# Kernel optimization log

Measured on AMD Instinct MI355X. Metric: run time of the kernel, lower is better.

Reference implementation:

```python
import jax, jax.numpy as jnp
import numpy as np

WS = 7          # window_size
NH = 4          # num_heads
C = 128         # channels
N = WS * WS     # tokens per window = 49
BW = 4096       # number of windows total (batch * windows_per_image)
NW = 64         # windows per image (mask leading dim)


def _rel_pos_index(ws):
    coords = np.stack(np.meshgrid(np.arange(ws), np.arange(ws), indexing='ij'))
    cf = coords.reshape(2, -1)
    rel = (cf[:, :, None] - cf[:, None, :]).transpose(1, 2, 0)
    rel[:, :, 0] += ws - 1
    rel[:, :, 1] += ws - 1
    rel[:, :, 0] *= 2 * ws - 1
    return jnp.asarray(rel.sum(-1).ravel(), dtype=jnp.int32)  # [N*N]


def setup_inputs() -> dict:
    key = jax.random.key(0)
    ks = jax.random.split(key, 6)
    x = jax.random.normal(ks[0], (BW, N, C), dtype=jnp.float32)
    qkv_w = jax.random.normal(ks[1], (C, 3 * C), dtype=jnp.float32) * 0.02
    qkv_b = jnp.zeros((3 * C,), dtype=jnp.float32)
    proj_w = jax.random.normal(ks[2], (C, C), dtype=jnp.float32) * 0.02
    proj_b = jnp.zeros((C,), dtype=jnp.float32)
    bias_table = jax.random.normal(ks[3], ((2 * WS - 1) ** 2, NH), dtype=jnp.float32) * 0.02
    # Swin shifted-window mask: 0 where attention allowed, -100 where blocked
    keep = jax.random.bernoulli(ks[4], 0.5, (NW, N, N))
    mask = jnp.where(keep, 0.0, -100.0).astype(jnp.float32)
    return {"x": x, "qkv_w": qkv_w, "qkv_b": qkv_b, "proj_w": proj_w,
            "proj_b": proj_b, "bias_table": bias_table, "mask": mask}


def reference(x, qkv_w, qkv_b, proj_w, proj_b, bias_table, mask):
    B_, n, c = x.shape
    h = NH
    d = c // h
    scale = d ** -0.5

    qkv = x @ qkv_w + qkv_b                       # [B_, N, 3C]
    qkv = qkv.reshape(B_, n, 3, h, d).transpose(2, 0, 3, 1, 4)  # [3, B_, h, N, d]
    q, k, v = qkv[0], qkv[1], qkv[2]

    attn = jnp.einsum('bhnd,bhmd->bhnm', q * scale, k)          # [B_, h, N, N]

    idx = _rel_pos_index(WS)
    rpb = bias_table[idx].reshape(n, n, h).transpose(2, 0, 1)   # [h, N, N]
    attn = attn + rpb[None]

    nW = mask.shape[0]
    attn = attn.reshape(-1, nW, h, n, n) + mask[None, :, None]  # [B, nW, h, N, N]
    attn = attn.reshape(-1, h, n, n)
    attn = jax.nn.softmax(attn, axis=-1)

    out = jnp.einsum('bhnm,bhmd->bhnd', attn, v)  # [B_, h, N, d]
    out = out.transpose(0, 2, 1, 3).reshape(B_, n, c)
    return out @ proj_w + proj_b
```

## Files before the change

### kernel.cpp

```cpp
#include <hip/hip_runtime.h>

#define NTOK 49
#define CH   128
#define NHEAD 4
#define SCALE 0.17677669529663687f

typedef __bf16 bf16x8 __attribute__((ext_vector_type(8)));
typedef short  s16x8  __attribute__((ext_vector_type(8)));
typedef float  f32x4  __attribute__((ext_vector_type(4)));
typedef s16x8 s16x8_a __attribute__((may_alias));
typedef unsigned short u16_a __attribute__((may_alias));

__device__ __forceinline__ unsigned short f2bf(float f) {
  unsigned int u = __builtin_bit_cast(unsigned int, f);
  u += 0x7FFFu + ((u >> 16) & 1u);
  return (unsigned short)(u >> 16);
}

__device__ __forceinline__ f32x4 mfma_bf16(s16x8 a, s16x8 b, f32x4 c) {
  return __builtin_amdgcn_mfma_f32_16x16x32_bf16(
      __builtin_bit_cast(bf16x8, a), __builtin_bit_cast(bf16x8, b), c, 0, 0, 0);
}

__global__ void prep_kernel(const float* __restrict__ qkv_w,
                            const float* __restrict__ proj_w,
                            const float* __restrict__ bias_table,
                            unsigned short* __restrict__ wT,
                            unsigned short* __restrict__ pT,
                            float* __restrict__ rpb) {
  int t = blockIdx.x * 256 + threadIdx.x;
  if (t < 384 * 128) {
    int n = t >> 7, k = t & 127;
    float v = qkv_w[k * 384 + n];
    if (n < 128) v *= SCALE;
    wT[n * 128 + k] = f2bf(v);
  } else if (t < 384 * 128 + 128 * 128) {
    int u = t - 384 * 128;
    int n = u >> 7, k = u & 127;
    pT[n * 128 + k] = f2bf(proj_w[k * 128 + n]);
  } else if (t < 384 * 128 + 128 * 128 + NHEAD * NTOK * NTOK) {
    int u = t - (384 * 128 + 128 * 128);
    int h = u / (NTOK * NTOK);
    int ij = u % (NTOK * NTOK);
    int i = ij / NTOK, j = ij % NTOK;
    int idx = (i / 7 - j / 7 + 6) * 13 + (i % 7 - j % 7 + 6);
    rpb[h * (NTOK * NTOK) + ij] = bias_table[idx * NHEAD + h];
  }
}

__global__ __launch_bounds__(256, 3)
void attn_fused_kernel(const float* __restrict__ x,
                       const float* __restrict__ qkv_b,
                       const float* __restrict__ proj_b,
                       const float* __restrict__ mask,
                       const unsigned short* __restrict__ wT,
                       const unsigned short* __restrict__ pT,
                       const float* __restrict__ rpb,
                       float* __restrict__ out) {
  __shared__ __align__(16) char smem_raw[52224];
  unsigned short* const smem = (unsigned short*)smem_raw;

  const int w    = blockIdx.x;
  const int tid  = threadIdx.x;
  const int wave = tid >> 6;
  const int lane = tid & 63;
  const int quad = lane >> 4;
  const int l16  = lane & 15;
  const int h    = wave;
  const int wq8  = quad * 8;

  unsigned short* const Xs   = smem;
  unsigned short* const priv = smem + 6656 + wave * 4864;
  unsigned short* const qs   = priv;
  unsigned short* const ks   = priv;
  unsigned short* const ps   = priv;
  unsigned short* const vt   = priv + 2560;
  unsigned short* const ao   = smem;

  const f32x4 fzero = {0.f, 0.f, 0.f, 0.f};

  {
    const float* xw = x + (size_t)w * (NTOK * CH);
    for (int t = tid; t < NTOK * 32; t += 256) {
      const int row = t >> 5;
      const int c4  = (t & 31) << 2;
      const float4 v = *(const float4*)(xw + row * CH + c4);
      ushort4 pk;
      pk.x = f2bf(v.x); pk.y = f2bf(v.y); pk.z = f2bf(v.z); pk.w = f2bf(v.w);
      *(ushort4*)(Xs + row * 136 + c4) = pk;
    }
  }
  __syncthreads();

  int xrow[4];
#pragma unroll
  for (int mt = 0; mt < 4; ++mt) {
    const int rr = mt * 16 + l16;
    xrow[mt] = (rr < NTOK ? rr : NTOK - 1) * 136;
  }

  f32x4 accq[4][2];
#pragma unroll
  for (int mt = 0; mt < 4; ++mt)
#pragma unroll
    for (int nt = 0; nt < 2; ++nt) accq[mt][nt] = fzero;
#pragma unroll
  for (int kt = 0; kt < 4; ++kt) {
    s16x8 a[4], bq[2];
#pragma unroll
    for (int mt = 0; mt < 4; ++mt)
      a[mt] = *(const s16x8*)(Xs + xrow[mt] + kt * 32 + wq8);
#pragma unroll
    for (int nt = 0; nt < 2; ++nt)
      bq[nt] = *(const s16x8*)(wT + (size_t)(h * 32 + nt * 16 + l16) * 128 + kt * 32 + wq8);
#pragma unroll
    for (int mt = 0; mt < 4; ++mt)
#pragma unroll
      for (int nt = 0; nt < 2; ++nt)
        accq[mt][nt] = mfma_bf16(a[mt], bq[nt], accq[mt][nt]);
  }
#pragma unroll
  for (int nt = 0; nt < 2; ++nt) {
    const int col = nt * 16 + l16;
    const float bq_ = qkv_b[h * 32 + col] * SCALE;
#pragma unroll
    for (int mt = 0; mt < 4; ++mt)
#pragma unroll
      for (int r = 0; r < 4; ++r)
        *(u16_a*)(qs + (mt * 16 + quad * 4 + r) * 40 + col) = f2bf(accq[mt][nt][r] + bq_);
  }
  asm volatile("" ::: "memory");
  s16x8 qf[4];
#pragma unroll
  for (int t4 = 0; t4 < 4; ++t4)
    qf[t4] = *(const s16x8_a*)(qs + (t4 * 16 + l16) * 40 + wq8);
  asm volatile("s_waitcnt lgkmcnt(0)" ::: "memory");
  __builtin_amdgcn_sched_barrier(0);

  f32x4 acck[4][2];
#pragma unroll
  for (int mt = 0; mt < 4; ++mt)
#pragma unroll
    for (int nt = 0; nt < 2; ++nt) acck[mt][nt] = fzero;
#pragma unroll
  for (int kt = 0; kt < 4; ++kt) {
    s16x8 a[4], bk[2];
#pragma unroll
    for (int mt = 0; mt < 4; ++mt)
      a[mt] = *(const s16x8*)(Xs + xrow[mt] + kt * 32 + wq8);
#pragma unroll
    for (int nt = 0; nt < 2; ++nt)
      bk[nt] = *(const s16x8*)(wT + (size_t)(128 + h * 32 + nt * 16 + l16) * 128 + kt * 32 + wq8);
#pragma unroll
    for (int mt = 0; mt < 4; ++mt)
#pragma unroll
      for (int nt = 0; nt < 2; ++nt)
        acck[mt][nt] = mfma_bf16(a[mt], bk[nt], acck[mt][nt]);
  }
#pragma unroll
  for (int nt = 0; nt < 2; ++nt) {
    const int col = nt * 16 + l16;
    const float bk_ = qkv_b[128 + h * 32 + col];
#pragma unroll
    for (int mt = 0; mt < 4; ++mt)
#pragma unroll
      for (int r = 0; r < 4; ++r)
        *(u16_a*)(ks + (mt * 16 + quad * 4 + r) * 40 + col) = f2bf(acck[mt][nt][r] + bk_);
  }
  asm volatile("" ::: "memory");
  s16x8 kf[4];
#pragma unroll
  for (int t4 = 0; t4 < 4; ++t4)
    kf[t4] = *(const s16x8_a*)(ks + (t4 * 16 + l16) * 40 + wq8);
  asm volatile("s_waitcnt lgkmcnt(0)" ::: "memory");
  __builtin_amdgcn_sched_barrier(0);

  f32x4 accv[4][2];
#pragma unroll
  for (int mt = 0; mt < 4; ++mt)
#pragma unroll
    for (int nt = 0; nt < 2; ++nt) accv[mt][nt] = fzero;
#pragma unroll
  for (int kt = 0; kt < 4; ++kt) {
    s16x8 a[4], bv[2];
#pragma unroll
    for (int mt = 0; mt < 4; ++mt)
      a[mt] = *(const s16x8*)(Xs + xrow[mt] + kt * 32 + wq8);
#pragma unroll
    for (int nt = 0; nt < 2; ++nt)
      bv[nt] = *(const s16x8*)(wT + (size_t)(256 + h * 32 + nt * 16 + l16) * 128 + kt * 32 + wq8);
#pragma unroll
    for (int mt = 0; mt < 4; ++mt)
#pragma unroll
      for (int nt = 0; nt < 2; ++nt)
        accv[mt][nt] = mfma_bf16(a[mt], bv[nt], accv[mt][nt]);
  }
#pragma unroll
  for (int nt = 0; nt < 2; ++nt) {
    const float bv_ = qkv_b[256 + h * 32 + nt * 16 + l16];
#pragma unroll
    for (int mt = 0; mt < 4; ++mt)
#pragma unroll
      for (int r = 0; r < 4; ++r) {
        const int row = mt * 16 + quad * 4 + r;
        const int col = nt * 16 + l16;
        *(u16_a*)(vt + col * 72 + row) = f2bf(accv[mt][nt][r] + bv_);
      }
  }

  f32x4 s[4][4];
#pragma unroll
  for (int mt = 0; mt < 4; ++mt)
#pragma unroll
    for (int nt = 0; nt < 4; ++nt)
      s[mt][nt] = mfma_bf16(qf[mt], kf[nt], fzero);

  const float* maskw = mask + (size_t)(w & 63) * (NTOK * NTOK);
  const float* rpbh  = rpb + h * (NTOK * NTOK);
  float rinv[4][4];
  unsigned int pHold[4][4];
#pragma unroll
  for (int mt = 0; mt < 4; ++mt) {
#pragma unroll
    for (int r = 0; r < 4; ++r) {
      const int i = mt * 16 + quad * 4 + r;
      float vals[4];
      float vmax = -1e30f;
#pragma unroll
      for (int nt = 0; nt < 4; ++nt) {
        const int j = nt * 16 + l16;
        float v = -1e30f;
        if (i < NTOK && j < NTOK) {
          const int ij = i * NTOK + j;
          v = s[mt][nt][r] + rpbh[ij] + maskw[ij];
        }
        vals[nt] = v;
        vmax = fmaxf(vmax, v);
      }
#pragma unroll
      for (int off = 1; off < 16; off <<= 1)
        vmax = fmaxf(vmax, __shfl_xor(vmax, off, 64));
      float rsum = 0.f;
#pragma unroll
      for (int nt = 0; nt < 4; ++nt) {
        const float e = __expf(vals[nt] - vmax);
        vals[nt] = e;
        rsum += e;
      }
#pragma unroll
      for (int off = 1; off < 16; off <<= 1)
        rsum += __shfl_xor(rsum, off, 64);
      rinv[mt][r] = 1.f / rsum;
      *(u16_a*)(ps + i * 40 + l16)      = f2bf(vals[0]);
      *(u16_a*)(ps + i * 40 + 16 + l16) = f2bf(vals[1]);
      pHold[mt][r] = (unsigned int)f2bf(vals[2]) | ((unsigned int)f2bf(vals[3]) << 16);
    }
  }

  f32x4 o[4][2];
#pragma unroll
  for (int mt = 0; mt < 4; ++mt)
#pragma unroll
    for (int nt = 0; nt < 2; ++nt) o[mt][nt] = fzero;
  {
    s16x8 pf[4], vf[2];
#pragma unroll
    for (int mt = 0; mt < 4; ++mt)
      pf[mt] = *(const s16x8_a*)(ps + (mt * 16 + l16) * 40 + wq8);
#pragma unroll
    for (int nt = 0; nt < 2; ++nt)
      vf[nt] = *(const s16x8_a*)(vt + (nt * 16 + l16) * 72 + wq8);
#pragma unroll
    for (int mt = 0; mt < 4; ++mt)
#pragma unroll
      for (int nt = 0; nt < 2; ++nt)
        o[mt][nt] = mfma_bf16(pf[mt], vf[nt], o[mt][nt]);
  }
  asm volatile("s_waitcnt lgkmcnt(0)" ::: "memory");
  __builtin_amdgcn_sched_barrier(0);
#pragma unroll
  for (int mt = 0; mt < 4; ++mt)
#pragma unroll
    for (int r = 0; r < 4; ++r) {
      const int i = mt * 16 + quad * 4 + r;
      *(u16_a*)(ps + i * 40 + l16)      = (unsigned short)(pHold[mt][r] & 0xFFFFu);
      *(u16_a*)(ps + i * 40 + 16 + l16) = (unsigned short)(pHold[mt][r] >> 16);
    }
  asm volatile("" ::: "memory");
  {
    s16x8 pf[4], vf[2];
#pragma unroll
    for (int mt = 0; mt < 4; ++mt)
      pf[mt] = *(const s16x8_a*)(ps + (mt * 16 + l16) * 40 + wq8);
#pragma unroll
    for (int nt = 0; nt < 2; ++nt)
      vf[nt] = *(const s16x8_a*)(vt + (nt * 16 + l16) * 72 + 32 + wq8);
#pragma unroll
    for (int mt = 0; mt < 4; ++mt)
#pragma unroll
      for (int nt = 0; nt < 2; ++nt)
        o[mt][nt] = mfma_bf16(pf[mt], vf[nt], o[mt][nt]);
  }

  __syncthreads();
#pragma unroll
  for (int mt = 0; mt < 4; ++mt)
#pragma unroll
    for (int nt = 0; nt < 2; ++nt)
#pragma unroll
      for (int r = 0; r < 4; ++r) {
        const int row = mt * 16 + quad * 4 + r;
        *(u16_a*)(ao + row * 136 + h * 32 + nt * 16 + l16) = f2bf(o[mt][nt][r] * rinv[mt][r]);
      }
  __syncthreads();

  f32x4 po[4][2];
#pragma unroll
  for (int mt = 0; mt < 4; ++mt)
#pragma unroll
    for (int nt = 0; nt < 2; ++nt) po[mt][nt] = fzero;
#pragma unroll
  for (int kt = 0; kt < 4; ++kt) {
    s16x8 a[4], b[2];
#pragma unroll
    for (int mt = 0; mt < 4; ++mt)
      a[mt] = *(const s16x8_a*)(ao + (mt * 16 + l16) * 136 + kt * 32 + wq8);
#pragma unroll
    for (int nt = 0; nt < 2; ++nt)
      b[nt] = *(const s16x8*)(pT + (size_t)(h * 32 + nt * 16 + l16) * 128 + kt * 32 + wq8);
#pragma unroll
    for (int mt = 0; mt < 4; ++mt)
#pragma unroll
      for (int nt = 0; nt < 2; ++nt)
        po[mt][nt] = mfma_bf16(a[mt], b[nt], po[mt][nt]);
  }
  float* outw = out + (size_t)w * (NTOK * CH);
#pragma unroll
  for (int nt = 0; nt < 2; ++nt) {
    const int col = h * 32 + nt * 16 + l16;
    const float pb = proj_b[col];
#pragma unroll
    for (int mt = 0; mt < 4; ++mt)
#pragma unroll
      for (int r = 0; r < 4; ++r) {
        const int row = mt * 16 + quad * 4 + r;
        if (row < NTOK) outw[row * CH + col] = po[mt][nt][r] + pb;
      }
  }
}

extern "C" void kernel_launch(void* const* d_in, const int* in_sizes, int n_in,
                              void* d_out, int out_size, void* d_ws, size_t ws_size,
                              hipStream_t stream) {
  (void)in_sizes; (void)n_in; (void)out_size; (void)ws_size;
  const float* x          = (const float*)d_in[0];
  const float* qkv_w      = (const float*)d_in[1];
  const float* qkv_b      = (const float*)d_in[2];
  const float* proj_w     = (const float*)d_in[3];
  const float* proj_b     = (const float*)d_in[4];
  const float* bias_table = (const float*)d_in[5];
  const float* mask       = (const float*)d_in[6];
  float* out = (float*)d_out;

  unsigned short* wT = (unsigned short*)d_ws;
  unsigned short* pT = wT + 384 * 128;
  float* rpb = (float*)(pT + 128 * 128);

  const int prep_items = 384 * 128 + 128 * 128 + NHEAD * NTOK * NTOK;
  prep_kernel<<<(prep_items + 255) / 256, 256, 0, stream>>>(qkv_w, proj_w, bias_table,
                                                            wT, pT, rpb);
  attn_fused_kernel<<<4096, 256, 0, stream>>>(x, qkv_b, proj_b, mask, wT, pT, rpb, out);
}
```

Measured before the change: 294.8 us.

## Load x fragments directly from global memory and drop shared staging

Removes the shared-memory staging of the window's input rows. Each wave now loads its MFMA A-fragments straight from global fp32 x and converts them to bf16 in registers, once each for the Q, K and V projections. This frees about 13 KB of LDS per block and removes a block-wide barrier, and launch bounds are raised to target 4 resident blocks per CU. In exchange, every wave re-reads the whole window's x from cache three times and repeats the fp32-to-bf16 conversion, which multiplies global/L2 load traffic and ALU work.

```diff
diff --git a/kernel.cpp b/kernel.cpp
--- a/kernel.cpp
+++ b/kernel.cpp
@@ -48,7 +48,7 @@
   }
 }
 
-__global__ __launch_bounds__(256, 3)
+__global__ __launch_bounds__(256, 4)
 void attn_fused_kernel(const float* __restrict__ x,
                        const float* __restrict__ qkv_b,
                        const float* __restrict__ proj_b,
@@ -57,7 +57,7 @@
                        const unsigned short* __restrict__ pT,
                        const float* __restrict__ rpb,
                        float* __restrict__ out) {
-  __shared__ __align__(16) char smem_raw[52224];
+  __shared__ __align__(16) char smem_raw[38912];
   unsigned short* const smem = (unsigned short*)smem_raw;
 
   const int w    = blockIdx.x;
@@ -69,8 +69,7 @@
   const int h    = wave;
   const int wq8  = quad * 8;
 
-  unsigned short* const Xs   = smem;
-  unsigned short* const priv = smem + 6656 + wave * 4864;
+  unsigned short* const priv = smem + wave * 4864;
   unsigned short* const qs   = priv;
   unsigned short* const ks   = priv;
   unsigned short* const ps   = priv;
@@ -79,24 +78,12 @@
 
   const f32x4 fzero = {0.f, 0.f, 0.f, 0.f};
 
-  {
-    const float* xw = x + (size_t)w * (NTOK * CH);
-    for (int t = tid; t < NTOK * 32; t += 256) {
-      const int row = t >> 5;
-      const int c4  = (t & 31) << 2;
-      const float4 v = *(const float4*)(xw + row * CH + c4);
-      ushort4 pk;
-      pk.x = f2bf(v.x); pk.y = f2bf(v.y); pk.z = f2bf(v.z); pk.w = f2bf(v.w);
-      *(ushort4*)(Xs + row * 136 + c4) = pk;
-    }
-  }
-  __syncthreads();
-
-  int xrow[4];
+  const float* xw = x + (size_t)w * (NTOK * CH);
+  int rofs[4];
 #pragma unroll
   for (int mt = 0; mt < 4; ++mt) {
     const int rr = mt * 16 + l16;
-    xrow[mt] = (rr < NTOK ? rr : NTOK - 1) * 136;
+    rofs[mt] = (rr < NTOK ? rr : NTOK - 1) * CH;
   }
 
   f32x4 accq[4][2];
@@ -108,8 +95,15 @@
   for (int kt = 0; kt < 4; ++kt) {
     s16x8 a[4], bq[2];
 #pragma unroll
-    for (int mt = 0; mt < 4; ++mt)
-      a[mt] = *(const s16x8*)(Xs + xrow[mt] + kt * 32 + wq8);
+    for (int mt = 0; mt < 4; ++mt) {
+      const float* pa = xw + rofs[mt] + kt * 32 + wq8;
+      const float4 f0 = *(const float4*)pa;
+      const float4 f1 = *(const float4*)(pa + 4);
+      union { s16x8 v; unsigned short s[8]; } ua;
+      ua.s[0] = f2bf(f0.x); ua.s[1] = f2bf(f0.y); ua.s[2] = f2bf(f0.z); ua.s[3] = f2bf(f0.w);
+      ua.s[4] = f2bf(f1.x); ua.s[5] = f2bf(f1.y); ua.s[6] = f2bf(f1.z); ua.s[7] = f2bf(f1.w);
+      a[mt] = ua.v;
+    }
 #pragma unroll
     for (int nt = 0; nt < 2; ++nt)
       bq[nt] = *(const s16x8*)(wT + (size_t)(h * 32 + nt * 16 + l16) * 128 + kt * 32 + wq8);
@@ -146,8 +140,15 @@
   for (int kt = 0; kt < 4; ++kt) {
     s16x8 a[4], bk[2];
 #pragma unroll
-    for (int mt = 0; mt < 4; ++mt)
-      a[mt] = *(const s16x8*)(Xs + xrow[mt] + kt * 32 + wq8);
+    for (int mt = 0; mt < 4; ++mt) {
+      const float* pa = xw + rofs[mt] + kt * 32 + wq8;
+      const float4 f0 = *(const float4*)pa;
+      const float4 f1 = *(const float4*)(pa + 4);
+      union { s16x8 v; unsigned short s[8]; } ua;
+      ua.s[0] = f2bf(f0.x); ua.s[1] = f2bf(f0.y); ua.s[2] = f2bf(f0.z); ua.s[3] = f2bf(f0.w);
+      ua.s[4] = f2bf(f1.x); ua.s[5] = f2bf(f1.y); ua.s[6] = f2bf(f1.z); ua.s[7] = f2bf(f1.w);
+      a[mt] = ua.v;
+    }
 #pragma unroll
     for (int nt = 0; nt < 2; ++nt)
       bk[nt] = *(const s16x8*)(wT + (size_t)(128 + h * 32 + nt * 16 + l16) * 128 + kt * 32 + wq8);
@@ -184,8 +185,15 @@
   for (int kt = 0; kt < 4; ++kt) {
     s16x8 a[4], bv[2];
 #pragma unroll
-    for (int mt = 0; mt < 4; ++mt)
-      a[mt] = *(const s16x8*)(Xs + xrow[mt] + kt * 32 + wq8);
+    for (int mt = 0; mt < 4; ++mt) {
+      const float* pa = xw + rofs[mt] + kt * 32 + wq8;
+      const float4 f0 = *(const float4*)pa;
+      const float4 f1 = *(const float4*)(pa + 4);
+      union { s16x8 v; unsigned short s[8]; } ua;
+      ua.s[0] = f2bf(f0.x); ua.s[1] = f2bf(f0.y); ua.s[2] = f2bf(f0.z); ua.s[3] = f2bf(f0.w);
+      ua.s[4] = f2bf(f1.x); ua.s[5] = f2bf(f1.y); ua.s[6] = f2bf(f1.z); ua.s[7] = f2bf(f1.w);
+      a[mt] = ua.v;
+    }
 #pragma unroll
     for (int nt = 0; nt < 2; ++nt)
       bv[nt] = *(const s16x8*)(wT + (size_t)(256 + h * 32 + nt * 16 + l16) * 128 + kt * 32 + wq8);
```

Result: slower. 444.3 us (+50.7%).
